# Performance work log

Hardware: AMD Instinct MI355X
Metric: run time of the kernel (lower is better)

## Reference

```python
import jax, jax.numpy as jnp
import numpy as np

N, E, D, H = 50000, 800000, 128, 8
DH = D // H
EPS = 1e-12


def setup_inputs() -> dict:
    key = jax.random.key(0)
    ks = jax.random.split(key, 12)
    s = 0.02
    return {
        "h": jax.random.normal(ks[0], (N, D), jnp.float32),
        "Wq": jax.random.normal(ks[1], (D, D), jnp.float32) * s,
        "bq": jax.random.normal(ks[2], (D,), jnp.float32) * s,
        "Wk": jax.random.normal(ks[3], (D, D), jnp.float32) * s,
        "bk": jax.random.normal(ks[4], (D,), jnp.float32) * s,
        "Wv": jax.random.normal(ks[5], (D, D), jnp.float32) * s,
        "bv": jax.random.normal(ks[6], (D,), jnp.float32) * s,
        "Wo": jax.random.normal(ks[7], (D, D), jnp.float32) * s,
        "bo": jax.random.normal(ks[8], (D,), jnp.float32) * s,
        "gamma": jnp.ones((D,), jnp.float32),
        "beta": jnp.zeros((D,), jnp.float32),
        "src": jax.random.randint(ks[9], (E,), 0, N, jnp.int32),
        "dst": jax.random.randint(ks[10], (E,), 0, N, jnp.int32),
    }


def reference(h, Wq, bq, Wk, bk, Wv, bv, Wo, bo, gamma, beta, src, dst):
    n = h.shape[0]
    # node-wise projections, split into heads: [N, H, DH]
    Q = (h @ Wq + bq).reshape(n, H, DH)
    K = (h @ Wk + bk).reshape(n, H, DH)
    V = (h @ Wv + bv).reshape(n, H, DH)
    # edge-wise scores: sum over head dim of K[src] * Q[dst] -> [E, H]
    scores = jnp.sum(K[src] * Q[dst], axis=-1)
    # edge softmax, normalized over incoming edges of each dst node
    m = jax.lax.stop_gradient(jax.ops.segment_max(scores, dst, num_segments=n))
    ex = jnp.exp(scores - m[dst])
    denom = jax.ops.segment_sum(ex, dst, num_segments=n)
    p = ex / denom[dst]  # [E, H]
    # weighted message + scatter-sum aggregate -> [N, H, DH]
    msg = V[src] * p[:, :, None]
    agg = jax.ops.segment_sum(msg, dst, num_segments=n).reshape(n, D)
    # BertSelfOutput: dense + residual + layernorm (dropout is identity in eval)
    y = agg @ Wo + bo + h
    mu = jnp.mean(y, axis=-1, keepdims=True)
    var = jnp.mean(jnp.square(y - mu), axis=-1, keepdims=True)
    out = (y - mu) / jnp.sqrt(var + EPS) * gamma + beta
    return out
```

## Files before the change

### kernel.cpp

```cpp
#include <hip/hip_runtime.h>
#include <hip/hip_bf16.h>
#include <math.h>

#define D 128
#define EPS 1e-12f
#define CPAD 16

typedef __attribute__((ext_vector_type(8))) short bf16x8;
typedef __attribute__((ext_vector_type(4))) float f32x4;
typedef __attribute__((ext_vector_type(2))) float f32x2;

__device__ __forceinline__ unsigned short f2bf(float f) {
    unsigned int u = __float_as_uint(f);
    return (unsigned short)((u + 0x7fffu + ((u >> 16) & 1u)) >> 16);
}
__device__ __forceinline__ float bf2f_lo(unsigned int packed) {
    return __uint_as_float(packed << 16);
}
__device__ __forceinline__ float bf2f_hi(unsigned int packed) {
    return __uint_as_float(packed & 0xffff0000u);
}
__device__ __forceinline__ unsigned char f2fp8(float f) {
    return (unsigned char)__builtin_amdgcn_cvt_pk_fp8_f32(f, f, 0, false);
}

__global__ __launch_bounds__(256) void prep_kernel(
    const float* __restrict__ Wq, const float* __restrict__ Wk,
    const float* __restrict__ Wv, const float* __restrict__ Wo,
    unsigned short* __restrict__ WT,
    const int* __restrict__ dst, int* __restrict__ counts,
    int* __restrict__ ticket, int E) {
    int bx = blockIdx.x;
    int tid = threadIdx.x;
    if (bx < 64) {
        __shared__ unsigned short tile[32][33];
        int m = bx >> 4;
        int t = bx & 15;
        const float* W = (m == 0) ? Wq : (m == 1) ? Wk : (m == 2) ? Wv : Wo;
        int r0 = (t & 3) * 32;
        int c0 = (t >> 2) * 32;
        int row = tid >> 3, c4 = (tid & 7) * 4;
        float4 v = *(const float4*)&W[(size_t)(r0 + row) * D + c0 + c4];
        tile[c4 + 0][row] = f2bf(v.x);
        tile[c4 + 1][row] = f2bf(v.y);
        tile[c4 + 2][row] = f2bf(v.z);
        tile[c4 + 3][row] = f2bf(v.w);
        __syncthreads();
        unsigned int lo = (unsigned int)tile[row][c4] | ((unsigned int)tile[row][c4 + 1] << 16);
        unsigned int hi = (unsigned int)tile[row][c4 + 2] | ((unsigned int)tile[row][c4 + 3] << 16);
        uint2 pk; pk.x = lo; pk.y = hi;
        int n = c0 + row;
        int ct = n >> 4, l15 = n & 15;
        int ks = t & 3;
        int quad = c4 >> 3;
        int j = c4 & 7;
        size_t off = (size_t)m * 16384 + (size_t)(((ct * 4 + ks) * 64) + quad * 16 + l15) * 8 + j;
        *(uint2*)&WT[off] = pk;
    } else {
        int e = ((bx - 64) * 256 + tid) * 4;
        if (e >= E) return;
        if (e + 3 < E) {
            int4 d4 = *(const int4*)&dst[e];
            int4 t4;
            t4.x = atomicAdd(&counts[d4.x * CPAD], 1);
            t4.y = atomicAdd(&counts[d4.y * CPAD], 1);
            t4.z = atomicAdd(&counts[d4.z * CPAD], 1);
            t4.w = atomicAdd(&counts[d4.w * CPAD], 1);
            *(int4*)&ticket[e] = t4;
        } else {
            for (int i = e; i < E; ++i) ticket[i] = atomicAdd(&counts[dst[i] * CPAD], 1);
        }
    }
}

__device__ __forceinline__ int block_incl_scan256(int v, int tid, int* wsum) {
    int lane = tid & 63;
    int wid = tid >> 6;
#pragma unroll
    for (int off = 1; off < 64; off <<= 1) {
        int t = __shfl_up(v, off, 64);
        if (lane >= off) v += t;
    }
    if (lane == 63) wsum[wid] = v;
    __syncthreads();
#pragma unroll
    for (int w = 0; w < 4; ++w)
        if (w < wid) v += wsum[w];
    return v;
}

__global__ void scan1_kernel(const int* __restrict__ counts, int* __restrict__ offsets,
                             int* __restrict__ chunksum, int n) {
    __shared__ int wsum[4];
    int tid = threadIdx.x;
    int i = blockIdx.x * 256 + tid;
    int v = (i < n) ? counts[i * CPAD] : 0;
    int incl = block_incl_scan256(v, tid, wsum);
    if (i < n) offsets[i + 1] = incl;
    if (tid == 255) chunksum[blockIdx.x] = incl;
}

__global__ void scan2_kernel(const int* __restrict__ chunksum, int* __restrict__ chunkbase, int nchunks) {
    __shared__ int wsum[4];
    int tid = threadIdx.x;
    int v = (tid < nchunks) ? chunksum[tid] : 0;
    int incl = block_incl_scan256(v, tid, wsum);
    if (tid < nchunks) chunkbase[tid] = incl - v;
}

__global__ void scan3_kernel(int* __restrict__ offsets, const int* __restrict__ chunkbase, int n) {
    int i = blockIdx.x * 256 + threadIdx.x;
    if (i < n) {
        offsets[i + 1] += chunkbase[blockIdx.x];
        if (i == 0) offsets[0] = 0;
    }
}

__global__ __launch_bounds__(256) void fill_qkv_kernel(
    const int* __restrict__ dst, const int* __restrict__ src,
    const int* __restrict__ ticket, const int* __restrict__ offsets,
    int* __restrict__ psrc, int E, int e4blocks,
    const float* __restrict__ h, const unsigned short* __restrict__ WT,
    const float* __restrict__ bq, const float* __restrict__ bk, const float* __restrict__ bv,
    unsigned short* __restrict__ Qb, unsigned char* __restrict__ K8,
    unsigned char* __restrict__ V8, int n) {
    __shared__ __align__(16) unsigned short wt[16384];
    int bx = blockIdx.x;
    int tid = threadIdx.x;
    if (bx < e4blocks) {
        int e = (bx * 256 + tid) * 4;
        if (e >= E) return;
        if (e + 3 < E) {
            int4 d4 = *(const int4*)&dst[e];
            int4 s4 = *(const int4*)&src[e];
            int4 t4 = *(const int4*)&ticket[e];
            psrc[offsets[d4.x] + t4.x] = s4.x;
            psrc[offsets[d4.y] + t4.y] = s4.y;
            psrc[offsets[d4.z] + t4.z] = s4.z;
            psrc[offsets[d4.w] + t4.w] = s4.w;
        } else {
            for (int i = e; i < E; ++i) psrc[offsets[dst[i]] + ticket[i]] = src[i];
        }
        return;
    }
    int bid = bx - e4blocks;
    int lane = tid & 63, wave = tid >> 6;
    int quad = lane >> 4, l15 = lane & 15;
    int rt = bid * 64 + wave * 16;

    int rowA = min(rt + l15, n - 1);
    bf16x8 af[4];
#pragma unroll
    for (int ks = 0; ks < 4; ++ks) {
        const float* ap = &h[(size_t)rowA * D + ks * 32 + quad * 8];
        float4 a0 = *(const float4*)ap;
        float4 a1 = *(const float4*)(ap + 4);
        union { unsigned short u[8]; bf16x8 v; } pk;
        pk.u[0] = f2bf(a0.x); pk.u[1] = f2bf(a0.y);
        pk.u[2] = f2bf(a0.z); pk.u[3] = f2bf(a0.w);
        pk.u[4] = f2bf(a1.x); pk.u[5] = f2bf(a1.y);
        pk.u[6] = f2bf(a1.z); pk.u[7] = f2bf(a1.w);
        af[ks] = pk.v;
    }

    for (int m = 0; m < 3; ++m) {
#pragma unroll
        for (int it = 0; it < 8; ++it) {
            int idx = it * 256 + tid;
            *(uint4*)&wt[idx * 8] = *(const uint4*)&WT[(size_t)m * 16384 + idx * 8];
        }
        __syncthreads();

        f32x4 acc[8];
#pragma unroll
        for (int ct = 0; ct < 8; ++ct) {
            acc[ct] = (f32x4){0.f, 0.f, 0.f, 0.f};
#pragma unroll
            for (int ks = 0; ks < 4; ++ks) {
                bf16x8 bfr = *(const bf16x8*)&wt[((ct * 4 + ks) * 64 + lane) * 8];
                acc[ct] = __builtin_amdgcn_mfma_f32_16x16x32_bf16(af[ks], bfr, acc[ct], 0, 0, 0);
            }
        }
        __syncthreads();

        const float* bias = (m == 0) ? bq : (m == 1) ? bk : bv;
#pragma unroll
        for (int ct = 0; ct < 8; ++ct) {
            int col = ct * 16 + l15;
            float bb = bias[col];
#pragma unroll
            for (int r = 0; r < 4; ++r) {
                int row = rt + quad * 4 + r;
                if (row < n) {
                    float v = acc[ct][r] + bb;
                    if (m == 0)      Qb[(size_t)row * D + col] = f2bf(v);
                    else if (m == 1) K8[(size_t)row * D + col] = f2fp8(v);
                    else             V8[(size_t)row * D + col] = f2fp8(v);
                }
            }
        }
    }
}

__global__ __launch_bounds__(256) void edge_attn_kernel(
    const unsigned short* __restrict__ Qb, const unsigned char* __restrict__ K8,
    const unsigned char* __restrict__ V8,
    const int* __restrict__ offsets, const int* __restrict__ psrc,
    unsigned short* __restrict__ aggb, int n) {
    int wave = (blockIdx.x * 256 + threadIdx.x) >> 6;
    int lane = threadIdx.x & 63;
    if (wave >= n) return;
    int start = offsets[wave], end = offsets[wave + 1];
    int j = lane >> 3, hd = lane & 7;

    const unsigned short* qp = &Qb[(size_t)wave * D + hd * 16];
    uint4 qa = *(const uint4*)qp;
    uint4 qb = *(const uint4*)(qp + 8);
    float q[16];
    q[0] = bf2f_lo(qa.x);  q[1] = bf2f_hi(qa.x);
    q[2] = bf2f_lo(qa.y);  q[3] = bf2f_hi(qa.y);
    q[4] = bf2f_lo(qa.z);  q[5] = bf2f_hi(qa.z);
    q[6] = bf2f_lo(qa.w);  q[7] = bf2f_hi(qa.w);
    q[8] = bf2f_lo(qb.x);  q[9] = bf2f_hi(qb.x);
    q[10] = bf2f_lo(qb.y); q[11] = bf2f_hi(qb.y);
    q[12] = bf2f_lo(qb.z); q[13] = bf2f_hi(qb.z);
    q[14] = bf2f_lo(qb.w); q[15] = bf2f_hi(qb.w);

    float l = 0.f;
    float acc[16] = {};

    if (start < end) {
        int s = psrc[min(start + j, end - 1)];
        for (int base = start; base < end; base += 8) {
            uint4 ku = *(const uint4*)&K8[(size_t)s * D + hd * 16];
            uint4 vu = *(const uint4*)&V8[(size_t)s * D + hd * 16];
            int nb = base + 8;
            int sn = (nb < end) ? psrc[min(nb + j, end - 1)] : 0;
            bool valid = (base + j) < end;

            float kf[16], vf[16];
            {
                f32x2 t;
                t = __builtin_amdgcn_cvt_pk_f32_fp8(ku.x, false); kf[0] = t.x;  kf[1] = t.y;
                t = __builtin_amdgcn_cvt_pk_f32_fp8(ku.x, true);  kf[2] = t.x;  kf[3] = t.y;
                t = __builtin_amdgcn_cvt_pk_f32_fp8(ku.y, false); kf[4] = t.x;  kf[5] = t.y;
                t = __builtin_amdgcn_cvt_pk_f32_fp8(ku.y, true);  kf[6] = t.x;  kf[7] = t.y;
                t = __builtin_amdgcn_cvt_pk_f32_fp8(ku.z, false); kf[8] = t.x;  kf[9] = t.y;
                t = __builtin_amdgcn_cvt_pk_f32_fp8(ku.z, true);  kf[10] = t.x; kf[11] = t.y;
                t = __builtin_amdgcn_cvt_pk_f32_fp8(ku.w, false); kf[12] = t.x; kf[13] = t.y;
                t = __builtin_amdgcn_cvt_pk_f32_fp8(ku.w, true);  kf[14] = t.x; kf[15] = t.y;
                t = __builtin_amdgcn_cvt_pk_f32_fp8(vu.x, false); vf[0] = t.x;  vf[1] = t.y;
                t = __builtin_amdgcn_cvt_pk_f32_fp8(vu.x, true);  vf[2] = t.x;  vf[3] = t.y;
                t = __builtin_amdgcn_cvt_pk_f32_fp8(vu.y, false); vf[4] = t.x;  vf[5] = t.y;
                t = __builtin_amdgcn_cvt_pk_f32_fp8(vu.y, true);  vf[6] = t.x;  vf[7] = t.y;
                t = __builtin_amdgcn_cvt_pk_f32_fp8(vu.z, false); vf[8] = t.x;  vf[9] = t.y;
                t = __builtin_amdgcn_cvt_pk_f32_fp8(vu.z, true);  vf[10] = t.x; vf[11] = t.y;
                t = __builtin_amdgcn_cvt_pk_f32_fp8(vu.w, false); vf[12] = t.x; vf[13] = t.y;
                t = __builtin_amdgcn_cvt_pk_f32_fp8(vu.w, true);  vf[14] = t.x; vf[15] = t.y;
            }

            float sc = q[0] * kf[0];
#pragma unroll
            for (int i = 1; i < 16; ++i) sc = fmaf(q[i], kf[i], sc);

            float p = valid ? __expf(sc) : 0.f;
            l += p;
#pragma unroll
            for (int i = 0; i < 16; ++i) acc[i] = fmaf(p, vf[i], acc[i]);
            s = sn;
        }
    }

#pragma unroll
    for (int off = 8; off <= 32; off <<= 1) {
        l += __shfl_xor(l, off, 64);
#pragma unroll
        for (int i = 0; i < 16; ++i) acc[i] += __shfl_xor(acc[i], off, 64);
    }
    float inv = (l > 0.f) ? 1.f / l : 0.f;
    if (j == 0) {
        uint4 o0, o1;
        o0.x = (unsigned int)f2bf(acc[0] * inv) | ((unsigned int)f2bf(acc[1] * inv) << 16);
        o0.y = (unsigned int)f2bf(acc[2] * inv) | ((unsigned int)f2bf(acc[3] * inv) << 16);
        o0.z = (unsigned int)f2bf(acc[4] * inv) | ((unsigned int)f2bf(acc[5] * inv) << 16);
        o0.w = (unsigned int)f2bf(acc[6] * inv) | ((unsigned int)f2bf(acc[7] * inv) << 16);
        o1.x = (unsigned int)f2bf(acc[8] * inv) | ((unsigned int)f2bf(acc[9] * inv) << 16);
        o1.y = (unsigned int)f2bf(acc[10] * inv) | ((unsigned int)f2bf(acc[11] * inv) << 16);
        o1.z = (unsigned int)f2bf(acc[12] * inv) | ((unsigned int)f2bf(acc[13] * inv) << 16);
        o1.w = (unsigned int)f2bf(acc[14] * inv) | ((unsigned int)f2bf(acc[15] * inv) << 16);
        unsigned short* op = &aggb[(size_t)wave * D + hd * 16];
        *(uint4*)op = o0;
        *(uint4*)(op + 8) = o1;
    }
}

__global__ __launch_bounds__(256) void out_ln_mfma_kernel(
    const unsigned short* __restrict__ aggb, const unsigned short* __restrict__ WTo,
    const float* __restrict__ bo, const float* __restrict__ hres,
    const float* __restrict__ gamma, const float* __restrict__ beta,
    float* __restrict__ out, int n) {
    int tid = threadIdx.x;
    int lane = tid & 63, wave = tid >> 6;
    int quad = lane >> 4, l15 = lane & 15;
    int rt = blockIdx.x * 64 + wave * 16;

    int rowA = min(rt + l15, n - 1);
    bf16x8 af[4];
#pragma unroll
    for (int ks = 0; ks < 4; ++ks)
        af[ks] = *(const bf16x8*)&aggb[(size_t)rowA * D + ks * 32 + quad * 8];

    f32x4 acc[8];
#pragma unroll
    for (int ct = 0; ct < 8; ++ct) {
        acc[ct] = (f32x4){0.f, 0.f, 0.f, 0.f};
#pragma unroll
        for (int ks = 0; ks < 4; ++ks) {
            bf16x8 bfr = *(const bf16x8*)&WTo[(size_t)((ct * 4 + ks) * 64 + lane) * 8];
            acc[ct] = __builtin_amdgcn_mfma_f32_16x16x32_bf16(af[ks], bfr, acc[ct], 0, 0, 0);
        }
    }

    float bb[8], gg[8], be[8];
#pragma unroll
    for (int ct = 0; ct < 8; ++ct) {
        int col = ct * 16 + l15;
        bb[ct] = bo[col];
        gg[ct] = gamma[col];
        be[ct] = beta[col];
    }
#pragma unroll
    for (int ct = 0; ct < 8; ++ct) {
        int col = ct * 16 + l15;
#pragma unroll
        for (int r = 0; r < 4; ++r) {
            int row = rt + quad * 4 + r;
            float hv = (row < n) ? hres[(size_t)row * D + col] : 0.f;
            acc[ct][r] = acc[ct][r] + bb[ct] + hv;
        }
    }

#pragma unroll
    for (int r = 0; r < 4; ++r) {
        float s1 = 0.f, s2 = 0.f;
#pragma unroll
        for (int ct = 0; ct < 8; ++ct) {
            float v = acc[ct][r];
            s1 += v;
            s2 += v * v;
        }
        s1 += __shfl_xor(s1, 1, 64); s2 += __shfl_xor(s2, 1, 64);
        s1 += __shfl_xor(s1, 2, 64); s2 += __shfl_xor(s2, 2, 64);
        s1 += __shfl_xor(s1, 4, 64); s2 += __shfl_xor(s2, 4, 64);
        s1 += __shfl_xor(s1, 8, 64); s2 += __shfl_xor(s2, 8, 64);
        float mu = s1 * (1.f / 128.f);
        float var = s2 * (1.f / 128.f) - mu * mu;
        float rs = rsqrtf(fmaxf(var, 0.f) + EPS);
        int row = rt + quad * 4 + r;
        if (row < n) {
#pragma unroll
            for (int ct = 0; ct < 8; ++ct) {
                int col = ct * 16 + l15;
                out[(size_t)row * D + col] = (acc[ct][r] - mu) * rs * gg[ct] + be[ct];
            }
        }
    }
}

extern "C" void kernel_launch(void* const* d_in, const int* in_sizes, int n_in,
                              void* d_out, int out_size, void* d_ws, size_t ws_size,
                              hipStream_t stream) {
    const float* h     = (const float*)d_in[0];
    const float* Wq    = (const float*)d_in[1];
    const float* bq    = (const float*)d_in[2];
    const float* Wk    = (const float*)d_in[3];
    const float* bk    = (const float*)d_in[4];
    const float* Wv    = (const float*)d_in[5];
    const float* bv    = (const float*)d_in[6];
    const float* Wo    = (const float*)d_in[7];
    const float* bo    = (const float*)d_in[8];
    const float* gamma = (const float*)d_in[9];
    const float* beta  = (const float*)d_in[10];
    const int* src     = (const int*)d_in[11];
    const int* dst     = (const int*)d_in[12];
    float* out = (float*)d_out;

    int N = in_sizes[0] / D;
    int E = in_sizes[11];

    unsigned short* Qb = (unsigned short*)d_ws;
    unsigned short* Ab = Qb + (size_t)N * D;
    unsigned short* WT = Ab + (size_t)N * D;
    unsigned char* K8  = (unsigned char*)(WT + 4 * D * D);
    unsigned char* V8  = K8 + (size_t)N * D;
    int* counts   = (int*)(V8 + (size_t)N * D);
    int* offsets  = counts + (size_t)N * CPAD;
    int* chunksum = offsets + (N + 1);
    int* chunkbase = chunksum + 256;
    int* ticket   = chunkbase + 256;
    int* psrc     = ticket + E;

    int nchunks = (N + 255) / 256;
    int e4blocks = ((E + 3) / 4 + 255) / 256;
    int nqkv = (N + 63) / 64;

    hipMemsetAsync(counts, 0, (size_t)N * CPAD * sizeof(int), stream);
    prep_kernel<<<64 + e4blocks, 256, 0, stream>>>(Wq, Wk, Wv, Wo, WT, dst, counts, ticket, E);
    scan1_kernel<<<nchunks, 256, 0, stream>>>(counts, offsets, chunksum, N);
    scan2_kernel<<<1, 256, 0, stream>>>(chunksum, chunkbase, nchunks);
    scan3_kernel<<<nchunks, 256, 0, stream>>>(offsets, chunkbase, N);
    fill_qkv_kernel<<<e4blocks + nqkv, 256, 0, stream>>>(
        dst, src, ticket, offsets, psrc, E, e4blocks,
        h, WT, bq, bk, bv, Qb, K8, V8, N);
    edge_attn_kernel<<<(N + 3) / 4, 256, 0, stream>>>(Qb, K8, V8, offsets, psrc, Ab, N);
    out_ln_mfma_kernel<<<(N + 63) / 64, 256, 0, stream>>>(Ab, WT + 3 * D * D, bo, h, gamma, beta, out, N);
}
```

Measured before the change: 222.4 us.

## Interleave K/V fp8 rows, process two nodes per wave, fuse scan passes

K and V fp8 projections are stored interleaved per node (256 bytes per row) so each edge gathers both from one contiguous region. The edge attention kernel now gives each node 32 lanes (4 edges per iteration) instead of a full wave, cutting idle lanes for the low average in-degree of about 16. The second and third scan kernels are merged, with each block summing the preceding chunk totals itself, which removes one launch. The trade-off is more loop iterations per node and redundant chunk-sum reads across blocks.

```diff
diff --git a/kernel.cpp b/kernel.cpp
--- a/kernel.cpp
+++ b/kernel.cpp
@@ -100,18 +100,19 @@
     if (tid == 255) chunksum[blockIdx.x] = incl;
 }
 
-__global__ void scan2_kernel(const int* __restrict__ chunksum, int* __restrict__ chunkbase, int nchunks) {
+__global__ void scan23_kernel(int* __restrict__ offsets, const int* __restrict__ chunksum, int n) {
     __shared__ int wsum[4];
-    int tid = threadIdx.x;
-    int v = (tid < nchunks) ? chunksum[tid] : 0;
-    int incl = block_incl_scan256(v, tid, wsum);
-    if (tid < nchunks) chunkbase[tid] = incl - v;
-}
-
-__global__ void scan3_kernel(int* __restrict__ offsets, const int* __restrict__ chunkbase, int n) {
-    int i = blockIdx.x * 256 + threadIdx.x;
+    int bx = blockIdx.x, tid = threadIdx.x;
+    int v = 0;
+    for (int t = tid; t < bx; t += 256) v += chunksum[t];
+#pragma unroll
+    for (int off = 32; off >= 1; off >>= 1) v += __shfl_xor(v, off, 64);
+    if ((tid & 63) == 0) wsum[tid >> 6] = v;
+    __syncthreads();
+    int base = wsum[0] + wsum[1] + wsum[2] + wsum[3];
+    int i = bx * 256 + tid;
     if (i < n) {
-        offsets[i + 1] += chunkbase[blockIdx.x];
+        offsets[i + 1] += base;
         if (i == 0) offsets[0] = 0;
     }
 }
@@ -122,8 +123,7 @@
     int* __restrict__ psrc, int E, int e4blocks,
     const float* __restrict__ h, const unsigned short* __restrict__ WT,
     const float* __restrict__ bq, const float* __restrict__ bk, const float* __restrict__ bv,
-    unsigned short* __restrict__ Qb, unsigned char* __restrict__ K8,
-    unsigned char* __restrict__ V8, int n) {
+    unsigned short* __restrict__ Qb, unsigned char* __restrict__ KV8, int n) {
     __shared__ __align__(16) unsigned short wt[16384];
     int bx = blockIdx.x;
     int tid = threadIdx.x;
@@ -194,8 +194,8 @@
                 if (row < n) {
                     float v = acc[ct][r] + bb;
                     if (m == 0)      Qb[(size_t)row * D + col] = f2bf(v);
-                    else if (m == 1) K8[(size_t)row * D + col] = f2fp8(v);
-                    else             V8[(size_t)row * D + col] = f2fp8(v);
+                    else if (m == 1) KV8[(size_t)row * 256 + col] = f2fp8(v);
+                    else             KV8[(size_t)row * 256 + 128 + col] = f2fp8(v);
                 }
             }
         }
@@ -203,17 +203,16 @@
 }
 
 __global__ __launch_bounds__(256) void edge_attn_kernel(
-    const unsigned short* __restrict__ Qb, const unsigned char* __restrict__ K8,
-    const unsigned char* __restrict__ V8,
+    const unsigned short* __restrict__ Qb, const unsigned char* __restrict__ KV8,
     const int* __restrict__ offsets, const int* __restrict__ psrc,
     unsigned short* __restrict__ aggb, int n) {
-    int wave = (blockIdx.x * 256 + threadIdx.x) >> 6;
-    int lane = threadIdx.x & 63;
-    if (wave >= n) return;
-    int start = offsets[wave], end = offsets[wave + 1];
-    int j = lane >> 3, hd = lane & 7;
-
-    const unsigned short* qp = &Qb[(size_t)wave * D + hd * 16];
+    int node = (blockIdx.x * 256 + threadIdx.x) >> 5;
+    int l32 = threadIdx.x & 31;
+    if (node >= n) return;
+    int start = offsets[node], end = offsets[node + 1];
+    int j = l32 >> 3, hd = l32 & 7;
+
+    const unsigned short* qp = &Qb[(size_t)node * D + hd * 16];
     uint4 qa = *(const uint4*)qp;
     uint4 qb = *(const uint4*)(qp + 8);
     float q[16];
@@ -231,10 +230,11 @@
 
     if (start < end) {
         int s = psrc[min(start + j, end - 1)];
-        for (int base = start; base < end; base += 8) {
-            uint4 ku = *(const uint4*)&K8[(size_t)s * D + hd * 16];
-            uint4 vu = *(const uint4*)&V8[(size_t)s * D + hd * 16];
-            int nb = base + 8;
+        for (int base = start; base < end; base += 4) {
+            const unsigned char* kvp = &KV8[(size_t)s * 256 + hd * 16];
+            uint4 ku = *(const uint4*)kvp;
+            uint4 vu = *(const uint4*)(kvp + 128);
+            int nb = base + 4;
             int sn = (nb < end) ? psrc[min(nb + j, end - 1)] : 0;
             bool valid = (base + j) < end;
 
@@ -272,7 +272,7 @@
     }
 
 #pragma unroll
-    for (int off = 8; off <= 32; off <<= 1) {
+    for (int off = 8; off <= 16; off <<= 1) {
         l += __shfl_xor(l, off, 64);
 #pragma unroll
         for (int i = 0; i < 16; ++i) acc[i] += __shfl_xor(acc[i], off, 64);
@@ -288,7 +288,7 @@
         o1.y = (unsigned int)f2bf(acc[10] * inv) | ((unsigned int)f2bf(acc[11] * inv) << 16);
         o1.z = (unsigned int)f2bf(acc[12] * inv) | ((unsigned int)f2bf(acc[13] * inv) << 16);
         o1.w = (unsigned int)f2bf(acc[14] * inv) | ((unsigned int)f2bf(acc[15] * inv) << 16);
-        unsigned short* op = &aggb[(size_t)wave * D + hd * 16];
+        unsigned short* op = &aggb[(size_t)node * D + hd * 16];
         *(uint4*)op = o0;
         *(uint4*)(op + 8) = o1;
     }
@@ -391,13 +391,11 @@
     unsigned short* Qb = (unsigned short*)d_ws;
     unsigned short* Ab = Qb + (size_t)N * D;
     unsigned short* WT = Ab + (size_t)N * D;
-    unsigned char* K8  = (unsigned char*)(WT + 4 * D * D);
-    unsigned char* V8  = K8 + (size_t)N * D;
-    int* counts   = (int*)(V8 + (size_t)N * D);
+    unsigned char* KV8 = (unsigned char*)(WT + 4 * D * D);
+    int* counts   = (int*)(KV8 + (size_t)N * 256);
     int* offsets  = counts + (size_t)N * CPAD;
     int* chunksum = offsets + (N + 1);
-    int* chunkbase = chunksum + 256;
-    int* ticket   = chunkbase + 256;
+    int* ticket   = chunksum + 256;
     int* psrc     = ticket + E;
 
     int nchunks = (N + 255) / 256;
@@ -407,11 +405,10 @@
     hipMemsetAsync(counts, 0, (size_t)N * CPAD * sizeof(int), stream);
     prep_kernel<<<64 + e4blocks, 256, 0, stream>>>(Wq, Wk, Wv, Wo, WT, dst, counts, ticket, E);
     scan1_kernel<<<nchunks, 256, 0, stream>>>(counts, offsets, chunksum, N);
-    scan2_kernel<<<1, 256, 0, stream>>>(chunksum, chunkbase, nchunks);
-    scan3_kernel<<<nchunks, 256, 0, stream>>>(offsets, chunkbase, N);
+    scan23_kernel<<<nchunks, 256, 0, stream>>>(offsets, chunksum, N);
     fill_qkv_kernel<<<e4blocks + nqkv, 256, 0, stream>>>(
         dst, src, ticket, offsets, psrc, E, e4blocks,
-        h, WT, bq, bk, bv, Qb, K8, V8, N);
-    edge_attn_kernel<<<(N + 3) / 4, 256, 0, stream>>>(Qb, K8, V8, offsets, psrc, Ab, N);
+        h, WT, bq, bk, bv, Qb, KV8, N);
+    edge_attn_kernel<<<(N + 7) / 8, 256, 0, stream>>>(Qb, KV8, offsets, psrc, Ab, N);
     out_ln_mfma_kernel<<<(N + 63) / 64, 256, 0, stream>>>(Ab, WT + 3 * D * D, bo, h, gamma, beta, out, N);
 }
```

New measurement: 219.7 us. About the same (-1.2%).
